# Kernel optimization log

Hardware: AMD Instinct MI355X
Metric: run time of the kernel (lower is better)

Reference implementation:

```python
import jax, jax.numpy as jnp
import numpy as np

LN_EPS = 1e-5


def _make_valid_boxes(key, shape):
    # boxes in [x_min, y_min, x_max, y_max] with min < max
    k1, k2 = jax.random.split(key)
    mins = jax.random.uniform(k1, shape, dtype=jnp.float32)            # [.., 2]
    sizes = jax.random.uniform(k2, shape, dtype=jnp.float32) * 0.2 + 1e-3
    return jnp.concatenate([mins, mins + sizes], axis=-1)


def setup_inputs() -> dict:
    key = jax.random.key(0)
    k_t, k_b, k_w = jax.random.split(key, 3)
    N, H = 100000, 768
    target = _make_valid_boxes(k_t, (2,))          # [4]
    ocr_boxes = _make_valid_boxes(k_b, (N, 2))     # [N, 4]
    W = jax.random.normal(k_w, (11, H), dtype=jnp.float32) * (1.0 / np.sqrt(11))
    b = jnp.zeros((H,), dtype=jnp.float32)
    ln_gamma = jnp.ones((H,), dtype=jnp.float32)
    ln_beta = jnp.zeros((H,), dtype=jnp.float32)
    return {"target": target, "ocr_boxes": ocr_boxes, "W": W, "b": b,
            "ln_gamma": ln_gamma, "ln_beta": ln_beta}


def _geo_features(target, boxes):
    # target: [4], boxes: [N, 4]  (x_min, y_min, x_max, y_max)
    tx0, ty0, tx1, ty1 = target[0], target[1], target[2], target[3]
    x0, y0, x1, y1 = boxes[:, 0], boxes[:, 1], boxes[:, 2], boxes[:, 3]
    N = boxes.shape[0]
    ones = jnp.ones((N,), boxes.dtype)

    # HeightWidthRelation: [w1, h1, w2, h2, |w1-w2|, |h1-h2|]
    w1, h1 = tx1 - tx0, ty1 - ty0
    w2, h2 = x1 - x0, y1 - y0
    hw = jnp.stack([w1 * ones, h1 * ones, w2, h2,
                    jnp.abs(w1 - w2), jnp.abs(h1 - h2)], axis=-1)   # [N, 6]

    # Centers
    c1x, c1y = (tx0 + tx1) * 0.5, (ty0 + ty1) * 0.5
    c2x, c2y = (x0 + x1) * 0.5, (y0 + y1) * 0.5
    dx, dy = c2x - c1x, c2y - c1y

    # DistanceRelation: L2 center distance
    dist = jnp.sqrt(dx * dx + dy * dy)                               # [N]

    # IoURelation
    overlap = (tx0 < x1) & (tx1 > x0) & (ty0 < y1) & (ty1 > y0)
    xi0, yi0 = jnp.maximum(tx0, x0), jnp.maximum(ty0, y0)
    xi1, yi1 = jnp.minimum(tx1, x1), jnp.minimum(ty1, y1)
    inter = jnp.where(overlap, (xi1 - xi0) * (yi1 - yi0), 0.0)       # [N]
    a1 = w1 * h1
    a2 = w2 * h2
    union = a1 + a2 - inter
    iou = jnp.stack([inter / union, inter / a1, inter / a2], axis=-1)  # [N, 3]

    # AngleRelation: atan2(|dy|, |dx|) degree bucket (degree in [0, 90])
    degree = jnp.arctan2(jnp.abs(dy), jnp.abs(dx)) * (180.0 / jnp.pi)
    bucket = jnp.where((degree > 22.5) & (degree <= 67.5), 1.0,
             jnp.where((degree > 67.5) & (degree <= 112.5), 2.0,
             jnp.where((degree > 112.5) & (degree <= 157.5), 3.0,
             jnp.where((degree > 157.5) & (degree <= 202.5), 4.0,
             jnp.where((degree > 202.5) & (degree <= 247.5), 5.0,
             jnp.where((degree > 247.5) & (degree <= 292.5), 6.0,
             jnp.where((degree > 292.5) & (degree <= 337.5), 7.0, 8.0)))))))

    return jnp.concatenate([hw, dist[:, None], iou, bucket[:, None]], axis=-1)  # [N, 11]


def reference(target, ocr_boxes, W, b, ln_gamma, ln_beta):
    feats = _geo_features(target, ocr_boxes)            # [N, 11]
    x = feats @ W + b                                   # [N, H]
    mean = jnp.mean(x, axis=-1, keepdims=True)
    var = jnp.mean(jnp.square(x - mean), axis=-1, keepdims=True)
    x = (x - mean) * jax.lax.rsqrt(var + LN_EPS) * ln_gamma + ln_beta
    return jax.nn.relu(x)
```

## Files before the change

### kernel.cpp

```cpp
#include <hip/hip_runtime.h>
#include <math.h>

#define H 768
#define LN_EPS 1e-5f
#define NTRIP 2048

typedef float nfloat4 __attribute__((ext_vector_type(4)));

__device__ __forceinline__ void geo_feats(
    const float4 bx,
    const float tx0, const float ty0, const float tx1, const float ty1,
    const float w1, const float h1, const float c1x, const float c1y,
    const float a1, const float ra1,
    float* __restrict__ v)
{
    const float tanA = 0.41421356237309503f;
    const float tanB = 2.41421356237309503f;
    const float x0 = bx.x, y0 = bx.y, x1 = bx.z, y1 = bx.w;
    const float w2 = x1 - x0, h2 = y1 - y0;
    v[0] = w2; v[1] = h2;
    v[2] = fabsf(w1 - w2); v[3] = fabsf(h1 - h2);
    const float c2x = (x0 + x1) * 0.5f, c2y = (y0 + y1) * 0.5f;
    const float dx = c2x - c1x, dy = c2y - c1y;
    v[4] = __builtin_amdgcn_sqrtf(dx * dx + dy * dy);
    const bool overlap = (tx0 < x1) && (tx1 > x0) && (ty0 < y1) && (ty1 > y0);
    const float xi0 = fmaxf(tx0, x0), yi0 = fmaxf(ty0, y0);
    const float xi1 = fminf(tx1, x1), yi1 = fminf(ty1, y1);
    const float inter = overlap ? (xi1 - xi0) * (yi1 - yi0) : 0.0f;
    const float a2 = w2 * h2;
    const float uni = a1 + a2 - inter;
    v[5] = inter * __builtin_amdgcn_rcpf(uni);
    v[6] = inter * ra1;
    v[7] = inter * __builtin_amdgcn_rcpf(a2);
    const float adx = fabsf(dx), ady = fabsf(dy);
    v[8] = (ady > adx * tanA) ? ((ady > adx * tanB) ? 2.0f : 1.0f) : 8.0f;
}

__global__ __launch_bounds__(256) void gram_kernel(
    const float* __restrict__ W,
    const float* __restrict__ bias,
    float* __restrict__ ws)
{
    const int i = blockIdx.x;
    const int tid = threadIdx.x;

    int p = 0, q = 0;
    const float* A;
    const float* B = nullptr;
    if (i < 78) {
        while ((p + 1) * (p + 2) / 2 <= i) ++p;
        q = i - p * (p + 1) / 2;
        A = (p < 11) ? (W + p * H) : bias;
        B = (q < 11) ? (W + q * H) : bias;
    } else {
        p = i - 78;
        A = (p < 11) ? (W + p * H) : bias;
    }

    float acc = 0.0f;
    if (B) {
        for (int c = tid; c < H; c += 256) acc += A[c] * B[c];
    } else {
        for (int c = tid; c < H; c += 256) acc += A[c];
    }

    #pragma unroll
    for (int off = 32; off >= 1; off >>= 1) acc += __shfl_xor(acc, off, 64);

    __shared__ float red[4];
    if ((tid & 63) == 0) red[tid >> 6] = acc;
    __syncthreads();
    if (tid == 0) {
        const float s = ((red[0] + red[1]) + (red[2] + red[3])) * (1.0f / H);
        if (i < 78) { ws[p * 12 + q] = s; ws[q * 12 + p] = s; }
        else        { ws[144 + p] = s; }
    }
}

__global__ __launch_bounds__(256) void stats_kernel(
    const float* __restrict__ target,
    const float* __restrict__ boxes,
    const float* __restrict__ ws,
    float2* __restrict__ stats,
    int N)
{
    const float tx0 = target[0], ty0 = target[1], tx1 = target[2], ty1 = target[3];
    const float w1 = tx1 - tx0, h1 = ty1 - ty0;
    const float c1x = (tx0 + tx1) * 0.5f, c1y = (ty0 + ty1) * 0.5f;
    const float a1 = w1 * h1;
    const float ra1 = 1.0f / a1;

    float Q[9][9], qlin[9], mlin[9];
    #pragma unroll
    for (int l = 0; l < 9; ++l)
        #pragma unroll
        for (int k = 0; k < 9; ++k)
            Q[l][k] = ws[(l + 2) * 12 + (k + 2)];
    #pragma unroll
    for (int k = 0; k < 9; ++k) {
        qlin[k] = 2.0f * (w1 * ws[0 * 12 + (k + 2)]
                        + h1 * ws[1 * 12 + (k + 2)]
                        +      ws[11 * 12 + (k + 2)]);
        mlin[k] = ws[144 + k + 2];
    }
    const float K = w1 * w1 * ws[0] + 2.0f * w1 * h1 * ws[1] + h1 * h1 * ws[13]
                  + 2.0f * w1 * ws[11] + 2.0f * h1 * ws[1 * 12 + 11] + ws[11 * 12 + 11];
    const float mconst = w1 * ws[144] + h1 * ws[145] + ws[155];

    const float4* __restrict__ boxes4 = reinterpret_cast<const float4*>(boxes);
    const int stride = gridDim.x * blockDim.x;
    for (int b = blockIdx.x * blockDim.x + threadIdx.x; b < N; b += stride) {
        const float4 bx = boxes4[b];
        float v[9];
        geo_feats(bx, tx0, ty0, tx1, ty1, w1, h1, c1x, c1y, a1, ra1, v);

        float mean = mconst;
        #pragma unroll
        for (int k = 0; k < 9; ++k) mean = fmaf(mlin[k], v[k], mean);

        float E = K;
        #pragma unroll
        for (int l = 0; l < 9; ++l) {
            float t = qlin[l];
            #pragma unroll
            for (int k = 0; k < 9; ++k) t = fmaf(Q[l][k], v[k], t);
            E = fmaf(t, v[l], E);
        }

        const float var  = fmaf(-mean, mean, E);
        const float rstd = __builtin_amdgcn_rsqf(fmaxf(var, 0.0f) + LN_EPS);
        float2 st; st.x = rstd; st.y = mean * rstd;
        stats[b] = st;
    }
}

__global__ __launch_bounds__(256, 4) void geo_ln_main(
    const float* __restrict__ target,
    const float* __restrict__ boxes,
    const float* __restrict__ W,
    const float* __restrict__ bias,
    const float* __restrict__ gamma,
    const float* __restrict__ beta,
    const float2* __restrict__ stats,
    float* __restrict__ out,
    int N)
{
    const int lane = threadIdx.x & 63;
    const int wl   = threadIdx.x >> 6;
    const int g    = (blockIdx.x << 2) | wl;
    const int t    = g / 3;
    const int role = g - 3 * t;

    const float tx0 = target[0], ty0 = target[1], tx1 = target[2], ty1 = target[3];
    const float w1 = tx1 - tx0, h1 = ty1 - ty0;
    const float c1x = (tx0 + tx1) * 0.5f, c1y = (ty0 + ty1) * 0.5f;
    const float a1 = w1 * h1;
    const float ra1 = 1.0f / a1;

    const float4* __restrict__ W4  = reinterpret_cast<const float4*>(W);
    const float4* __restrict__ b4  = reinterpret_cast<const float4*>(bias);
    const float4* __restrict__ g4  = reinterpret_cast<const float4*>(gamma);
    const float4* __restrict__ be4 = reinterpret_cast<const float4*>(beta);
    const float4* __restrict__ boxes4 = reinterpret_cast<const float4*>(boxes);
    nfloat4* __restrict__ outv = reinterpret_cast<nfloat4*>(out);

    const int c4 = lane + (role << 6);
    float4 base = b4[c4];
    {
        const float4 w0  = W4[0 * (H / 4) + c4];
        const float4 w1r = W4[1 * (H / 4) + c4];
        base.x = fmaf(w1, w0.x, base.x); base.y = fmaf(w1, w0.y, base.y);
        base.z = fmaf(w1, w0.z, base.z); base.w = fmaf(w1, w0.w, base.w);
        base.x = fmaf(h1, w1r.x, base.x); base.y = fmaf(h1, w1r.y, base.y);
        base.z = fmaf(h1, w1r.z, base.z); base.w = fmaf(h1, w1r.w, base.w);
    }
    float4 Wr[9];
    #pragma unroll
    for (int k = 0; k < 9; ++k) Wr[k] = W4[(k + 2) * (H / 4) + c4];
    const float4 gm = g4[c4];
    const float4 bt = be4[c4];

    __shared__ float recs[4][64 * 8];
    const int nb = (t < N) ? ((N - t + NTRIP - 1) / NTRIP) : 0;
    for (int l = lane; l < nb; l += 64) {
        const int b = t + l * NTRIP;
        const float4 bx = boxes4[b];
        const float2 st = stats[b];
        float* r = &recs[wl][l * 8];
        r[0] = bx.x; r[1] = bx.y; r[2] = bx.z; r[3] = bx.w;
        r[4] = st.x; r[5] = st.y;
    }
    __syncthreads();

    const float* rw = recs[wl];
    nfloat4* op = outv + (size_t)t * (H / 4) + c4;
    const size_t ostep = (size_t)NTRIP * (H / 4);

    #pragma unroll 2
    for (int k = 0; k < nb; ++k) {
        const float4 bx = *reinterpret_cast<const float4*>(rw + k * 8);
        const float rstd = rw[k * 8 + 4];
        const float nmr  = -rw[k * 8 + 5];

        float v[9];
        geo_feats(bx, tx0, ty0, tx1, ty1, w1, h1, c1x, c1y, a1, ra1, v);

        float4 acc = base;
        #pragma unroll
        for (int j = 0; j < 9; ++j) {
            const float4 w = Wr[j];
            acc.x = fmaf(v[j], w.x, acc.x);
            acc.y = fmaf(v[j], w.y, acc.y);
            acc.z = fmaf(v[j], w.z, acc.z);
            acc.w = fmaf(v[j], w.w, acc.w);
        }
        nfloat4 o;
        o.x = fmaxf(0.0f, fmaf(fmaf(acc.x, rstd, nmr), gm.x, bt.x));
        o.y = fmaxf(0.0f, fmaf(fmaf(acc.y, rstd, nmr), gm.y, bt.y));
        o.z = fmaxf(0.0f, fmaf(fmaf(acc.z, rstd, nmr), gm.z, bt.z));
        o.w = fmaxf(0.0f, fmaf(fmaf(acc.w, rstd, nmr), gm.w, bt.w));
        __builtin_nontemporal_store(o, op);
        op += ostep;
    }
}

__global__ __launch_bounds__(256, 2) void geo_ln_fallback(
    const float* __restrict__ target,
    const float* __restrict__ boxes,
    const float* __restrict__ W,
    const float* __restrict__ bias,
    const float* __restrict__ gamma,
    const float* __restrict__ beta,
    float* __restrict__ out,
    int N)
{
    const int lane = threadIdx.x & 63;
    const int wid  = (blockIdx.x << 2) | (threadIdx.x >> 6);
    const int nw   = gridDim.x << 2;

    const float tx0 = target[0], ty0 = target[1], tx1 = target[2], ty1 = target[3];
    const float w1 = tx1 - tx0, h1 = ty1 - ty0;
    const float c1x = (tx0 + tx1) * 0.5f, c1y = (ty0 + ty1) * 0.5f;
    const float a1 = w1 * h1;
    const float ra1 = 1.0f / a1;

    const float4* __restrict__ W4  = reinterpret_cast<const float4*>(W);
    const float4* __restrict__ b4  = reinterpret_cast<const float4*>(bias);
    const float4* __restrict__ g4  = reinterpret_cast<const float4*>(gamma);
    const float4* __restrict__ be4 = reinterpret_cast<const float4*>(beta);
    const float4* __restrict__ boxes4 = reinterpret_cast<const float4*>(boxes);
    nfloat4* __restrict__ outv = reinterpret_cast<nfloat4*>(out);

    float4 base[3], Wr[3][9], gm[3], bt[3];
    #pragma unroll
    for (int r = 0; r < 3; ++r) {
        const int c4 = lane + 64 * r;
        float4 acc = b4[c4];
        const float4 w0  = W4[0 * (H / 4) + c4];
        const float4 w1r = W4[1 * (H / 4) + c4];
        acc.x = fmaf(w1, w0.x, acc.x); acc.y = fmaf(w1, w0.y, acc.y);
        acc.z = fmaf(w1, w0.z, acc.z); acc.w = fmaf(w1, w0.w, acc.w);
        acc.x = fmaf(h1, w1r.x, acc.x); acc.y = fmaf(h1, w1r.y, acc.y);
        acc.z = fmaf(h1, w1r.z, acc.z); acc.w = fmaf(h1, w1r.w, acc.w);
        base[r] = acc;
        #pragma unroll
        for (int k = 0; k < 9; ++k)
            Wr[r][k] = W4[(k + 2) * (H / 4) + c4];
        gm[r] = g4[c4];
        bt[r] = be4[c4];
    }

    auto process = [&](int box) {
        const float4 bx = boxes4[box];
        float v[9];
        geo_feats(bx, tx0, ty0, tx1, ty1, w1, h1, c1x, c1y, a1, ra1, v);

        float4 xv[3];
        float s = 0.0f, sq = 0.0f;
        #pragma unroll
        for (int r = 0; r < 3; ++r) {
            float4 acc = base[r];
            #pragma unroll
            for (int k = 0; k < 9; ++k) {
                const float4 w = Wr[r][k];
                acc.x = fmaf(v[k], w.x, acc.x);
                acc.y = fmaf(v[k], w.y, acc.y);
                acc.z = fmaf(v[k], w.z, acc.z);
                acc.w = fmaf(v[k], w.w, acc.w);
            }
            xv[r] = acc;
            s  += acc.x + acc.y + acc.z + acc.w;
            sq += acc.x * acc.x + acc.y * acc.y + acc.z * acc.z + acc.w * acc.w;
        }

        #pragma unroll
        for (int off = 32; off >= 1; off >>= 1) {
            s  += __shfl_xor(s,  off, 64);
            sq += __shfl_xor(sq, off, 64);
        }
        const float mean = s * (1.0f / H);
        const float var  = sq * (1.0f / H) - mean * mean;
        const float rstd = __builtin_amdgcn_rsqf(var + LN_EPS);

        nfloat4* __restrict__ orow = outv + (size_t)box * (H / 4);
        #pragma unroll
        for (int r = 0; r < 3; ++r) {
            const float4 vx = xv[r];
            const float4 g = gm[r], be = bt[r];
            nfloat4 o;
            o.x = fmaxf(0.0f, (vx.x - mean) * rstd * g.x + be.x);
            o.y = fmaxf(0.0f, (vx.y - mean) * rstd * g.y + be.y);
            o.z = fmaxf(0.0f, (vx.z - mean) * rstd * g.z + be.z);
            o.w = fmaxf(0.0f, (vx.w - mean) * rstd * g.w + be.w);
            __builtin_nontemporal_store(o, &orow[lane + 64 * r]);
        }
    };

    int box = wid;
    for (; box + nw < N; box += 2 * nw) {
        process(box);
        process(box + nw);
    }
    if (box < N) process(box);
}

extern "C" void kernel_launch(void* const* d_in, const int* in_sizes, int n_in,
                              void* d_out, int out_size, void* d_ws, size_t ws_size,
                              hipStream_t stream) {
    const float* target = (const float*)d_in[0];
    const float* boxes  = (const float*)d_in[1];
    const float* W      = (const float*)d_in[2];
    const float* bias   = (const float*)d_in[3];
    const float* gamma  = (const float*)d_in[4];
    const float* beta   = (const float*)d_in[5];
    float* out = (float*)d_out;

    const int N = in_sizes[1] / 4;

    const size_t needed = (160 + 2 * (size_t)N) * sizeof(float);
    const bool stats_ok = d_ws && ws_size >= needed && N > 0 && N <= NTRIP * 64;

    if (stats_ok) {
        float* wsf = (float*)d_ws;
        float2* stats = (float2*)(wsf + 160);

        gram_kernel<<<90, 256, 0, stream>>>(W, bias, wsf);

        int blocksA2 = (N + 255) / 256;
        if (blocksA2 > 2048) blocksA2 = 2048;
        stats_kernel<<<blocksA2, 256, 0, stream>>>(target, boxes, wsf, stats, N);

        geo_ln_main<<<1536, 256, 0, stream>>>(target, boxes, W, bias, gamma, beta,
                                              stats, out, N);
    } else {
        geo_ln_fallback<<<512, 256, 0, stream>>>(target, boxes, W, bias, gamma, beta,
                                                 out, N);
    }
}
```

Measured before the change: 321.8 us.

## Stage output rows in LDS tiles and write them as contiguous blocks

The main kernel now gives each 192-thread block (three waves covering the 768 columns) a tile of 16 consecutive boxes, grid-striding over tiles. Results are computed into a shared-memory tile and then written out as a fully contiguous 48 KB region with nontemporal stores, instead of each wave writing one row segment per strided box. This aims to improve write coalescing and DRAM locality on the output, which dominates traffic. The cost is extra LDS traffic, two barriers per tile, and lower occupancy from the large LDS allocation and launch bounds of 2.

```diff
diff --git a/kernel.cpp b/kernel.cpp
--- a/kernel.cpp
+++ b/kernel.cpp
@@ -3,7 +3,9 @@
 
 #define H 768
 #define LN_EPS 1e-5f
-#define NTRIP 2048
+#define TILE 16
+#define TPB 192
+#define GRIDB 768
 
 typedef float nfloat4 __attribute__((ext_vector_type(4)));
 
@@ -134,7 +136,7 @@
     }
 }
 
-__global__ __launch_bounds__(256, 4) void geo_ln_main(
+__global__ __launch_bounds__(TPB, 2) void geo_ln_main(
     const float* __restrict__ target,
     const float* __restrict__ boxes,
     const float* __restrict__ W,
@@ -145,11 +147,9 @@
     float* __restrict__ out,
     int N)
 {
-    const int lane = threadIdx.x & 63;
-    const int wl   = threadIdx.x >> 6;
-    const int g    = (blockIdx.x << 2) | wl;
-    const int t    = g / 3;
-    const int role = g - 3 * t;
+    const int tid  = threadIdx.x;
+    const int lane = tid & 63;
+    const int role = tid >> 6;
 
     const float tx0 = target[0], ty0 = target[1], tx1 = target[2], ty1 = target[3];
     const float w1 = tx1 - tx0, h1 = ty1 - ty0;
@@ -180,47 +180,60 @@
     const float4 gm = g4[c4];
     const float4 bt = be4[c4];
 
-    __shared__ float recs[4][64 * 8];
-    const int nb = (t < N) ? ((N - t + NTRIP - 1) / NTRIP) : 0;
-    for (int l = lane; l < nb; l += 64) {
-        const int b = t + l * NTRIP;
-        const float4 bx = boxes4[b];
-        const float2 st = stats[b];
-        float* r = &recs[wl][l * 8];
-        r[0] = bx.x; r[1] = bx.y; r[2] = bx.z; r[3] = bx.w;
-        r[4] = st.x; r[5] = st.y;
-    }
-    __syncthreads();
-
-    const float* rw = recs[wl];
-    nfloat4* op = outv + (size_t)t * (H / 4) + c4;
-    const size_t ostep = (size_t)NTRIP * (H / 4);
-
-    #pragma unroll 2
-    for (int k = 0; k < nb; ++k) {
-        const float4 bx = *reinterpret_cast<const float4*>(rw + k * 8);
-        const float rstd = rw[k * 8 + 4];
-        const float nmr  = -rw[k * 8 + 5];
-
-        float v[9];
-        geo_feats(bx, tx0, ty0, tx1, ty1, w1, h1, c1x, c1y, a1, ra1, v);
-
-        float4 acc = base;
-        #pragma unroll
-        for (int j = 0; j < 9; ++j) {
-            const float4 w = Wr[j];
-            acc.x = fmaf(v[j], w.x, acc.x);
-            acc.y = fmaf(v[j], w.y, acc.y);
-            acc.z = fmaf(v[j], w.z, acc.z);
-            acc.w = fmaf(v[j], w.w, acc.w);
-        }
-        nfloat4 o;
-        o.x = fmaxf(0.0f, fmaf(fmaf(acc.x, rstd, nmr), gm.x, bt.x));
-        o.y = fmaxf(0.0f, fmaf(fmaf(acc.y, rstd, nmr), gm.y, bt.y));
-        o.z = fmaxf(0.0f, fmaf(fmaf(acc.z, rstd, nmr), gm.z, bt.z));
-        o.w = fmaxf(0.0f, fmaf(fmaf(acc.w, rstd, nmr), gm.w, bt.w));
-        __builtin_nontemporal_store(o, op);
-        op += ostep;
+    __shared__ float4 tileBuf[TILE * (H / 4)];
+    __shared__ float  recs[TILE * 8];
+
+    const int ntiles = (N + TILE - 1) / TILE;
+    for (int tl = blockIdx.x; tl < ntiles; tl += gridDim.x) {
+        const int b0  = tl * TILE;
+        const int nbx = (N - b0 < TILE) ? (N - b0) : TILE;
+
+        if (tid < nbx) {
+            const float4 bx = boxes4[b0 + tid];
+            const float2 st = stats[b0 + tid];
+            float* r = &recs[tid * 8];
+            r[0] = bx.x; r[1] = bx.y; r[2] = bx.z; r[3] = bx.w;
+            r[4] = st.x; r[5] = st.y;
+        }
+        __syncthreads();
+
+        for (int i = 0; i < nbx; ++i) {
+            const float4 bx  = *reinterpret_cast<const float4*>(&recs[i * 8]);
+            const float rstd = recs[i * 8 + 4];
+            const float nmr  = -recs[i * 8 + 5];
+
+            float v[9];
+            geo_feats(bx, tx0, ty0, tx1, ty1, w1, h1, c1x, c1y, a1, ra1, v);
+
+            float4 acc = base;
+            #pragma unroll
+            for (int j = 0; j < 9; ++j) {
+                const float4 w = Wr[j];
+                acc.x = fmaf(v[j], w.x, acc.x);
+                acc.y = fmaf(v[j], w.y, acc.y);
+                acc.z = fmaf(v[j], w.z, acc.z);
+                acc.w = fmaf(v[j], w.w, acc.w);
+            }
+            float4 o;
+            o.x = fmaxf(0.0f, fmaf(fmaf(acc.x, rstd, nmr), gm.x, bt.x));
+            o.y = fmaxf(0.0f, fmaf(fmaf(acc.y, rstd, nmr), gm.y, bt.y));
+            o.z = fmaxf(0.0f, fmaf(fmaf(acc.z, rstd, nmr), gm.z, bt.z));
+            o.w = fmaxf(0.0f, fmaf(fmaf(acc.w, rstd, nmr), gm.w, bt.w));
+            tileBuf[i * (H / 4) + c4] = o;
+        }
+        __syncthreads();
+
+        nfloat4* __restrict__ op = outv + (size_t)b0 * (H / 4);
+        const int nf4 = nbx * (H / 4);
+        #pragma unroll
+        for (int j = 0; j < TILE; ++j) {
+            const int idx = j * TPB + tid;
+            if (idx < nf4) {
+                const float4 o = tileBuf[idx];
+                nfloat4 no; no.x = o.x; no.y = o.y; no.z = o.z; no.w = o.w;
+                __builtin_nontemporal_store(no, &op[idx]);
+            }
+        }
     }
 }
 
@@ -338,7 +351,7 @@
     const int N = in_sizes[1] / 4;
 
     const size_t needed = (160 + 2 * (size_t)N) * sizeof(float);
-    const bool stats_ok = d_ws && ws_size >= needed && N > 0 && N <= NTRIP * 64;
+    const bool stats_ok = d_ws && ws_size >= needed && N > 0;
 
     if (stats_ok) {
         float* wsf = (float*)d_ws;
@@ -350,8 +363,8 @@
         if (blocksA2 > 2048) blocksA2 = 2048;
         stats_kernel<<<blocksA2, 256, 0, stream>>>(target, boxes, wsf, stats, N);
 
-        geo_ln_main<<<1536, 256, 0, stream>>>(target, boxes, W, bias, gamma, beta,
-                                              stats, out, N);
+        geo_ln_main<<<GRIDB, TPB, 0, stream>>>(target, boxes, W, bias, gamma, beta,
+                                               stats, out, N);
     } else {
         geo_ln_fallback<<<512, 256, 0, stream>>>(target, boxes, W, bias, gamma, beta,
                                                  out, N);
```

Result: slower. 331.6 us (+3.0%).
